# Kernel tuning notes

Measured on AMD Instinct MI355X. Metric: run time of the kernel, lower is better.

The kernel has to match this reference:

```python
import jax, jax.numpy as jnp
import numpy as np

NUM_HEADS = 16
EMBED_DIM = 2048
MAX_SEQ = 2048
HEAD_SIZE = EMBED_DIM // NUM_HEADS  # 128
ROPE_BASE = 10000.0


def setup_inputs() -> dict:
    key = jax.random.key(0)
    k1, k2, k3 = jax.random.split(key, 3)
    B, S = 4, 2048
    x = jax.random.normal(k1, (B, S, EMBED_DIM), dtype=jnp.float32)
    positions = jnp.arange(S, dtype=jnp.int32)
    # causal boolean mask: query i may attend to key j iff j <= i
    mask = jnp.tril(jnp.ones((S, MAX_SEQ), dtype=bool))[None, None]
    Wqkv = jax.random.normal(k2, (EMBED_DIM, 3 * EMBED_DIM), dtype=jnp.float32) * 0.02
    Wout = jax.random.normal(k3, (EMBED_DIM, EMBED_DIM), dtype=jnp.float32) * 0.02
    return {"x": x, "positions": positions, "mask": mask, "Wqkv": Wqkv, "Wout": Wout}


def _rope(x, positions):
    # x: [B, S, H, hd]; rotate interleaved (even, odd) pairs in last dim
    inv_freq = 1.0 / (ROPE_BASE ** (jnp.arange(0, HEAD_SIZE, 2, dtype=jnp.float32) / HEAD_SIZE))
    freq = positions.astype(jnp.float32)[:, None] * inv_freq[None, :]  # [S, hd/2]
    cos = jnp.cos(freq)[None, :, None, :]  # [1, S, 1, hd/2]
    sin = jnp.sin(freq)[None, :, None, :]
    xp = x.reshape(*x.shape[:-1], HEAD_SIZE // 2, 2)
    x0, x1 = xp[..., 0], xp[..., 1]
    out = jnp.stack([x0 * cos - x1 * sin, x1 * cos + x0 * sin], axis=-1)
    return out.reshape(x.shape)


def reference(x, positions, mask, Wqkv, Wout):
    B, S, D = x.shape
    H, hd = NUM_HEADS, HEAD_SIZE
    qkv = x @ Wqkv  # [B, S, 3D]
    q, k, v = jnp.split(qkv, 3, axis=-1)
    q = q.reshape(B, S, H, hd)
    k = k.reshape(B, S, H, hd)
    v = v.reshape(B, S, H, hd)
    q = _rope(q, positions)
    k = _rope(k, positions)
    # [B, H, S, hd]
    q = q.transpose(0, 2, 1, 3)
    k = k.transpose(0, 2, 1, 3)
    v = v.transpose(0, 2, 1, 3)
    # KV-cache update: write k/v at `positions` into a zero-initialized cache
    cache_k = jnp.zeros((B, H, MAX_SEQ, hd), dtype=x.dtype)
    cache_v = jnp.zeros((B, H, MAX_SEQ, hd), dtype=x.dtype)
    k = cache_k.at[:, :, positions].set(k)
    v = cache_v.at[:, :, positions].set(v)
    scale = 1.0 / jnp.sqrt(jnp.float32(hd))
    scores = jnp.einsum('bhqd,bhkd->bhqk', q, k) * scale  # [B, H, S, MAX_SEQ]
    scores = jnp.where(mask, scores, jnp.float32(-1e30))
    attn = jax.nn.softmax(scores, axis=-1)
    y = jnp.einsum('bhqk,bhkd->bhqd', attn, v)  # [B, H, S, hd]
    y = y.transpose(0, 2, 1, 3).reshape(B, S, D)
    return y @ Wout
```

## Files before the change

kernel.cpp:

```cpp
#include <hip/hip_runtime.h>
#include <hip/hip_bf16.h>
#include <cstdint>
#include <cstddef>

constexpr int CS = 2048;
constexpr int CHD = 128;
constexpr int CD = 2048;
constexpr int CN3 = 6144;

typedef __attribute__((ext_vector_type(8))) short short8;
typedef __attribute__((ext_vector_type(4))) float f32x4;

#define GLOAD_LDS16(g, l) __builtin_amdgcn_global_load_lds( \
    (const __attribute__((address_space(1))) void*)(g),      \
    (__attribute__((address_space(3))) void*)(l), 16, 0, 0)

__device__ __forceinline__ unsigned short f2bf(float f) {
  union { float f; unsigned u; } v; v.f = f;
  unsigned r = v.u + 0x7fffu + ((v.u >> 16) & 1u);
  return (unsigned short)(r >> 16);
}
__device__ __forceinline__ float bf2f(unsigned u16) {
  union { unsigned u; float f; } v; v.u = u16 << 16;
  return v.f;
}

template <int CTRL>
__device__ __forceinline__ float fmax_dpp(float x) {
  float y = __builtin_bit_cast(float, __builtin_amdgcn_update_dpp(
      __builtin_bit_cast(int, x), __builtin_bit_cast(int, x), CTRL, 0xf, 0xf, true));
  return fmaxf(x, y);
}
__device__ __forceinline__ float redmax16(float x) {
  x = fmax_dpp<0xB1>(x);
  x = fmax_dpp<0x4E>(x);
  x = fmax_dpp<0x141>(x);
  x = fmax_dpp<0x140>(x);
  return x;
}
__device__ __forceinline__ float dpp_xor1(float x) {
  return __builtin_bit_cast(float, __builtin_amdgcn_update_dpp(
      __builtin_bit_cast(int, x), __builtin_bit_cast(int, x), 0xB1, 0xf, 0xf, true));
}

__global__ __launch_bounds__(256) void k_cvt(const float* __restrict__ in,
                                             unsigned short* __restrict__ out, int n) {
  int i = (blockIdx.x * 256 + threadIdx.x) * 8;
  if (i >= n) return;
  float4 a = *(const float4*)(in + i);
  float4 b = *(const float4*)(in + i + 4);
  short8 o;
  o[0] = (short)f2bf(a.x); o[1] = (short)f2bf(a.y);
  o[2] = (short)f2bf(a.z); o[3] = (short)f2bf(a.w);
  o[4] = (short)f2bf(b.x); o[5] = (short)f2bf(b.y);
  o[6] = (short)f2bf(b.z); o[7] = (short)f2bf(b.w);
  *(short8*)(out + i) = o;
}

__global__ __launch_bounds__(256) void k_transcvt(const float* __restrict__ in,
                                                  unsigned short* __restrict__ out,
                                                  int R, int C) {
  __shared__ float tile[32][33];
  int c0 = blockIdx.x * 32, r0 = blockIdx.y * 32;
  int tx = threadIdx.x & 31, ty = threadIdx.x >> 5;
#pragma unroll
  for (int j = 0; j < 4; ++j)
    tile[ty + 8 * j][tx] = in[(size_t)(r0 + ty + 8 * j) * C + c0 + tx];
  __syncthreads();
#pragma unroll
  for (int j = 0; j < 4; ++j)
    out[(size_t)(c0 + ty + 8 * j) * R + r0 + tx] = f2bf(tile[tx][ty + 8 * j]);
}

__global__ __launch_bounds__(256) void k_vtrans(const unsigned short* __restrict__ V,
                                                unsigned short* __restrict__ Vt) {
  __shared__ unsigned short tile[32][33];
  int s0 = blockIdx.x * 32, d0 = blockIdx.y * 32, bh = blockIdx.z;
  int tx = threadIdx.x & 31, ty = threadIdx.x >> 5;
  const unsigned short* src = V + ((size_t)bh * CS + s0) * CHD + d0;
#pragma unroll
  for (int j = 0; j < 4; ++j)
    tile[ty + 8 * j][tx] = src[(size_t)(ty + 8 * j) * CHD + tx];
  __syncthreads();
  unsigned short* dst = Vt + ((size_t)bh * CHD + d0) * CS + s0;
#pragma unroll
  for (int j = 0; j < 4; ++j)
    dst[(size_t)(ty + 8 * j) * CS + tx] = tile[tx][ty + 8 * j];
}

__global__ void k_ropetab(float2* __restrict__ tab) {
  int p = blockIdx.x, c = threadIdx.x;
  float inv = powf(10000.0f, -(float)(2 * c) / 128.0f);
  float a = (float)p * inv;
  tab[p * 64 + c] = make_float2(cosf(a), sinf(a));
}

template <int EPI>
__global__ __launch_bounds__(512, 2) void k_gemm256(
    const unsigned short* __restrict__ A,
    const unsigned short* __restrict__ Bt,
    float* __restrict__ outF,
    unsigned short* __restrict__ outQ,
    unsigned short* __restrict__ outK,
    unsigned short* __restrict__ outV,
    const int* __restrict__ positions,
    const float2* __restrict__ tab,
    int M, int N, int K, int nbn) {
  const int nwg = gridDim.x;
  const int cpx = nwg >> 3;
  const int wg = blockIdx.x;
  const int swz = (wg & 7) * cpx + (wg >> 3);
  const int bn = swz % nbn, bm = swz / nbn;

  const int t = threadIdx.x;
  const int w = t >> 6, lane = t & 63;
  const int wr = w >> 2, wc = w & 3;
  const int lr = lane & 15, lg = lane >> 4;

  __shared__ char L[131072];

  const size_t Kb = (size_t)K * 2;
  const int srl = w * 16 + (lane >> 3);
  const int sch = ((lane & 7) ^ (lane >> 3)) * 16;
  const char* gA = (const char*)A + (size_t)(bm * 256 + srl) * Kb + sch;
  const char* gB = (const char*)Bt + (size_t)(bn * 256 + srl) * Kb + sch;
  const int ldst = w * 2048 + lane * 16;

#define STAGE(BUFB, OP, HALF, J, KT)                                               \
  GLOAD_LDS16(((OP) ? gB : gA) + (size_t)((HALF) * 128 + (J) * 8) * Kb +           \
                  (size_t)(KT) * 128,                                              \
              L + (BUFB) + (OP) * 32768 + (HALF) * 16384 + (J) * 1024 + ldst)

  const int xo = lr & 7;
  const int aRow = (wr * 128 + lr) * 128;
  const int bRow = (wc * 64 + lr) * 128;
#define RDA(BUFB, MI, KH) \
  (*(const short8*)(L + (BUFB) + aRow + (MI) * 2048 + ((((KH) * 4 + lg) ^ xo) << 4)))
#define RDB(BUFB, NI, KH) \
  (*(const short8*)(L + (BUFB) + 32768 + bRow + (NI) * 2048 + ((((KH) * 4 + lg) ^ xo) << 4)))

  f32x4 acc[8][4] = {};
  const int ktiles = K >> 6;

#pragma unroll
  for (int h = 0; h < 2; ++h)
#pragma unroll
    for (int j = 0; j < 2; ++j) { STAGE(0, 0, h, j, 0); STAGE(0, 1, h, j, 0); }
  if (ktiles > 1) {
    STAGE(65536, 0, 0, 0, 1); STAGE(65536, 0, 0, 1, 1);
    asm volatile("s_waitcnt vmcnt(2)" ::: "memory");
  } else {
    asm volatile("s_waitcnt vmcnt(0)" ::: "memory");
  }
  __builtin_amdgcn_s_barrier();

  short8 afr[4][2], bfr[4][2];

#define KTILE_PHASES(CB, NB, KT, DOSTAGE)                                          \
                                              \
  _Pragma("unroll") for (int mi = 0; mi < 4; ++mi)                                 \
      _Pragma("unroll") for (int kh = 0; kh < 2; ++kh)                             \
          afr[mi][kh] = RDA(CB, mi, kh);                                           \
  _Pragma("unroll") for (int ni = 0; ni < 2; ++ni)                                 \
      _Pragma("unroll") for (int kh = 0; kh < 2; ++kh)                             \
          bfr[ni][kh] = RDB(CB, ni, kh);                                           \
  if (DOSTAGE) { STAGE(NB, 0, 1, 0, (KT) + 1); STAGE(NB, 0, 1, 1, (KT) + 1); }     \
  __builtin_amdgcn_s_setprio(1);                                                   \
  _Pragma("unroll") for (int mi = 0; mi < 4; ++mi)                                 \
      _Pragma("unroll") for (int ni = 0; ni < 2; ++ni)                             \
          _Pragma("unroll") for (int kh = 0; kh < 2; ++kh)                         \
              acc[mi][ni] = __builtin_amdgcn_mfma_f32_16x16x32_bf16(               \
                  afr[mi][kh], bfr[ni][kh], acc[mi][ni], 0, 0, 0);                 \
  __builtin_amdgcn_s_setprio(0);                                                   \
                                                     \
  _Pragma("unroll") for (int ni = 2; ni < 4; ++ni)                                 \
      _Pragma("unroll") for (int kh = 0; kh < 2; ++kh)                             \
          bfr[ni][kh] = RDB(CB, ni, kh);                                           \
  if (DOSTAGE) { STAGE(NB, 1, 0, 0, (KT) + 1); STAGE(NB, 1, 0, 1, (KT) + 1); }     \
  __builtin_amdgcn_s_setprio(1);                                                   \
  _Pragma("unroll") for (int mi = 0; mi < 4; ++mi)                                 \
      _Pragma("unroll") for (int ni = 2; ni < 4; ++ni)                             \
          _Pragma("unroll") for (int kh = 0; kh < 2; ++kh)                         \
              acc[mi][ni] = __builtin_amdgcn_mfma_f32_16x16x32_bf16(               \
                  afr[mi][kh], bfr[ni][kh], acc[mi][ni], 0, 0, 0);                 \
  __builtin_amdgcn_s_setprio(0);                                                   \
                                                    \
  _Pragma("unroll") for (int mi = 0; mi < 4; ++mi)                                 \
      _Pragma("unroll") for (int kh = 0; kh < 2; ++kh)                             \
          afr[mi][kh] = RDA(CB, mi + 4, kh);                                       \
  if (DOSTAGE) { STAGE(NB, 1, 1, 0, (KT) + 1); STAGE(NB, 1, 1, 1, (KT) + 1); }     \
  __builtin_amdgcn_s_setprio(1);                                                   \
  _Pragma("unroll") for (int mi = 0; mi < 4; ++mi)                                 \
      _Pragma("unroll") for (int ni = 2; ni < 4; ++ni)                             \
          _Pragma("unroll") for (int kh = 0; kh < 2; ++kh)                         \
              acc[mi + 4][ni] = __builtin_amdgcn_mfma_f32_16x16x32_bf16(           \
                  afr[mi][kh], bfr[ni][kh], acc[mi + 4][ni], 0, 0, 0);             \
  __builtin_amdgcn_s_setprio(0);                                                   \
                                                       \
  __builtin_amdgcn_s_setprio(1);                                                   \
  _Pragma("unroll") for (int mi = 0; mi < 4; ++mi)                                 \
      _Pragma("unroll") for (int ni = 0; ni < 2; ++ni)                             \
          _Pragma("unroll") for (int kh = 0; kh < 2; ++kh)                         \
              acc[mi + 4][ni] = __builtin_amdgcn_mfma_f32_16x16x32_bf16(           \
                  afr[mi][kh], bfr[ni][kh], acc[mi + 4][ni], 0, 0, 0);             \
  __builtin_amdgcn_s_setprio(0);

  int c = 0;
  for (int kt = 0; kt < ktiles - 1; ++kt) {
    const int cb = c << 16, nb = (c ^ 1) << 16;
    KTILE_PHASES(cb, nb, kt, true)
    __builtin_amdgcn_s_barrier();
    if (kt + 2 < ktiles) {
      STAGE(cb, 0, 0, 0, kt + 2); STAGE(cb, 0, 0, 1, kt + 2);
      asm volatile("s_waitcnt vmcnt(2)" ::: "memory");
    } else {
      asm volatile("s_waitcnt vmcnt(0)" ::: "memory");
    }
    __builtin_amdgcn_s_barrier();
    c ^= 1;
  }
  {
    const int cb = c << 16, nb = 0;
    KTILE_PHASES(cb, nb, 0, false)
  }
#undef KTILE_PHASES
#undef STAGE
#undef RDA
#undef RDB

  if constexpr (EPI == 0) {
    const int which = bn >> 3;
    if (which < 2) {
      const float qsc = which ? 1.0f : 0.08838834764831845f;
      unsigned short* dstB = which ? outK : outQ;
#pragma unroll
      for (int mi = 0; mi < 8; ++mi)
#pragma unroll
        for (int rr = 0; rr < 4; ++rr) {
          int mg = bm * 256 + wr * 128 + mi * 16 + lg * 4 + rr;
          int bb = mg >> 11, s = mg & 2047;
          int pos = positions[s];
          int srow2 = which ? pos : s;
          const float2* tb = tab + pos * 64 + wc * 32 + (lr >> 1);
#pragma unroll
          for (int ni = 0; ni < 4; ++ni) {
            int cn = bn * 256 + wc * 64 + ni * 16 + lr;
            int h = (cn >> 7) & 15, d = cn & 127;
            float x = acc[mi][ni][rr];
            float p = dpp_xor1(x);
            float2 cs = tb[ni * 8];
            float y = (lr & 1) ? (x * cs.x + p * cs.y)
                               : (x * cs.x - p * cs.y);
            dstB[((size_t)(bb * 16 + h) * CS + srow2) * CHD + d] = f2bf(y * qsc);
          }
        }
    } else {
#pragma unroll
      for (int mi = 0; mi < 8; ++mi)
#pragma unroll
        for (int rr = 0; rr < 4; ++rr) {
          int mg = bm * 256 + wr * 128 + mi * 16 + lg * 4 + rr;
          int bb = mg >> 11, s = mg & 2047;
          int srow2 = positions[s];
#pragma unroll
          for (int ni = 0; ni < 4; ++ni) {
            int cn = bn * 256 + wc * 64 + ni * 16 + lr;
            int h = (cn >> 7) & 15, d = cn & 127;
            outV[((size_t)(bb * 16 + h) * CS + srow2) * CHD + d] = f2bf(acc[mi][ni][rr]);
          }
        }
    }
  } else {
#pragma unroll
    for (int mi = 0; mi < 8; ++mi)
#pragma unroll
      for (int rr = 0; rr < 4; ++rr) {
        int mg = bm * 256 + wr * 128 + mi * 16 + lg * 4 + rr;
#pragma unroll
        for (int ni = 0; ni < 4; ++ni)
          outF[(size_t)mg * N + bn * 256 + wc * 64 + ni * 16 + lr] = acc[mi][ni][rr];
      }
  }
}

__global__ __launch_bounds__(256, 3) void k_attn(
    const unsigned short* __restrict__ Q,
    const unsigned short* __restrict__ Kc,
    const unsigned short* __restrict__ Vt,
    unsigned short* __restrict__ Y) {
  const int qt_h = 15 - (blockIdx.x >> 6);
  const int bh = blockIdx.x & 63;
  const int q0 = qt_h * 128;
  const int t = threadIdx.x;
  const int w = t >> 6, lane = t & 63;
  const int lr = lane & 15, lg = lane >> 4;
  const int b = bh >> 4, h = bh & 15;

  __shared__ unsigned short lK[2][32 * 128];
  __shared__ unsigned short lVt[2][128 * 32];
  __shared__ unsigned short lP[4][32 * 40];

  const char* kg = (const char*)(Kc + (size_t)bh * CS * CHD);
  const char* vtg = (const char*)(Vt + (size_t)bh * CHD * CS);

  short8 qf[2][4];
#pragma unroll
  for (int qt = 0; qt < 2; ++qt)
#pragma unroll
    for (int ks = 0; ks < 4; ++ks)
      qf[qt][ks] = *(const short8*)(Q + ((size_t)bh * CS + q0 + w * 32 + qt * 16 + lr) * CHD + ks * 32 + lg * 8);

  f32x4 accy[2][8] = {};
  f32x4 accl[2] = {};
  float m[2][4];
#pragma unroll
  for (int qt = 0; qt < 2; ++qt)
#pragma unroll
    for (int r = 0; r < 4; ++r) m[qt][r] = -1e30f;

  short8 vone;
  {
    short o16 = (lr == 0) ? (short)0x3F80 : (short)0;
#pragma unroll
    for (int e = 0; e < 8; ++e) vone[e] = o16;
  }

  const int nch = 4 * qt_h + 4;
  const int qmaxw = q0 + w * 32 + 31;

  auto stage = [&](int ch) {
    const int kv0 = ch * 32;
    char* dK = (char*)lK[ch & 1];
    char* dV = (char*)lVt[ch & 1];
#pragma unroll
    for (int i = 0; i < 2; ++i) {
      int kr = w * 8 + i * 4 + lg;
      GLOAD_LDS16(kg + (size_t)(kv0 + kr) * 256 + ((lr * 16) ^ ((kr & 7) << 4)),
                  dK + w * 2048 + i * 1024 + lane * 16);
    }
#pragma unroll
    for (int i = 0; i < 2; ++i) {
      int vd = w * 32 + i * 16 + (lane >> 2);
      GLOAD_LDS16(vtg + (size_t)vd * 4096 + (size_t)kv0 * 2 + (lane & 3) * 16,
                  dV + w * 2048 + i * 1024 + lane * 16);
    }
  };

  stage(0);
  for (int ch = 0; ch < nch; ++ch) {
    __syncthreads();
    if (ch + 1 < nch) stage(ch + 1);

    const int kv0 = ch * 32;
    const unsigned short* bK = lK[ch & 1];
    const unsigned short* bV = lVt[ch & 1];

    if (kv0 <= qmaxw) {
      f32x4 sv[2][2] = {};
#pragma unroll
      for (int kvt = 0; kvt < 2; ++kvt) {
        short8 kf[4];
#pragma unroll
        for (int ks = 0; ks < 4; ++ks) {
          int row = kvt * 16 + lr;
          kf[ks] = *(const short8*)((const char*)bK + row * 256 + ((ks * 64 + lg * 16) ^ ((row & 7) << 4)));
        }
#pragma unroll
        for (int qt = 0; qt < 2; ++qt)
#pragma unroll
          for (int ks = 0; ks < 4; ++ks)
            sv[qt][kvt] = __builtin_amdgcn_mfma_f32_16x16x32_bf16(qf[qt][ks], kf[ks], sv[qt][kvt], 0, 0, 0);
      }
      float s0a[2][4], s1a[2][4], pm[2][4];
      bool need = false;
#pragma unroll
      for (int qt = 0; qt < 2; ++qt)
#pragma unroll
        for (int r = 0; r < 4; ++r) {
          const int qi = q0 + w * 32 + qt * 16 + lg * 4 + r;
          float s0 = (kv0 + lr <= qi) ? sv[qt][0][r] : -1e30f;
          float s1 = (kv0 + 16 + lr <= qi) ? sv[qt][1][r] : -1e30f;
          s0a[qt][r] = s0; s1a[qt][r] = s1;
          float mx = redmax16(fmaxf(s0, s1));
          pm[qt][r] = mx;
          need = need || (mx > m[qt][r] + 8.0f);
        }
      if (__any((int)need)) {
#pragma unroll
        for (int qt = 0; qt < 2; ++qt)
#pragma unroll
          for (int r = 0; r < 4; ++r) {
            float nm = fmaxf(m[qt][r], pm[qt][r]);
            float fr = __expf(m[qt][r] - nm);
            m[qt][r] = nm;
#pragma unroll
            for (int dt = 0; dt < 8; ++dt) accy[qt][dt][r] *= fr;
            accl[qt][r] *= fr;
          }
      }
      unsigned short* lp = lP[w];
#pragma unroll
      for (int qt = 0; qt < 2; ++qt)
#pragma unroll
        for (int r = 0; r < 4; ++r) {
          float p0 = __expf(s0a[qt][r] - m[qt][r]);
          float p1 = __expf(s1a[qt][r] - m[qt][r]);
          int prow = qt * 16 + lg * 4 + r;
          lp[prow * 40 + lr] = f2bf(p0);
          lp[prow * 40 + 16 + lr] = f2bf(p1);
        }
      short8 pa[2];
#pragma unroll
      for (int qt = 0; qt < 2; ++qt)
        pa[qt] = *(const short8*)(lp + (qt * 16 + lr) * 40 + lg * 8);
#pragma unroll
      for (int dt = 0; dt < 8; ++dt) {
        short8 vf = *(const short8*)((const char*)bV + (dt * 16 + lr) * 64 + lg * 16);
#pragma unroll
        for (int qt = 0; qt < 2; ++qt)
          accy[qt][dt] = __builtin_amdgcn_mfma_f32_16x16x32_bf16(pa[qt], vf, accy[qt][dt], 0, 0, 0);
      }
#pragma unroll
      for (int qt = 0; qt < 2; ++qt)
        accl[qt] = __builtin_amdgcn_mfma_f32_16x16x32_bf16(pa[qt], vone, accl[qt], 0, 0, 0);
    }
  }

#pragma unroll
  for (int qt = 0; qt < 2; ++qt)
#pragma unroll
    for (int r = 0; r < 4; ++r) {
      float lsum = accl[qt][r];
      lsum = __shfl(lsum, lane & 48, 64);
      float inv = 1.0f / lsum;
      int qrow = q0 + w * 32 + qt * 16 + lg * 4 + r;
      unsigned short* yr = Y + ((size_t)(b * CS + qrow)) * CD + h * CHD;
#pragma unroll
      for (int dt = 0; dt < 8; ++dt)
        yr[dt * 16 + lr] = f2bf(accy[qt][dt][r] * inv);
    }
}

extern "C" void kernel_launch(void* const* d_in, const int* in_sizes, int n_in,
                              void* d_out, int out_size, void* d_ws, size_t ws_size,
                              hipStream_t stream) {
  const float* x = (const float*)d_in[0];
  const int* positions = (const int*)d_in[1];
  const float* Wqkv = (const float*)d_in[3];
  const float* Wout = (const float*)d_in[4];
  float* out = (float*)d_out;

  char* ws = (char*)d_ws;
  size_t off = 0;
  auto alloc = [&](size_t bytes) {
    char* p = ws + off;
    off += (bytes + 255) & ~(size_t)255;
    return p;
  };
  unsigned short* q_bf = (unsigned short*)alloc((size_t)64 * CS * CHD * 2);
  unsigned short* k_bf = (unsigned short*)alloc((size_t)64 * CS * CHD * 2);
  unsigned short* v_bf = (unsigned short*)alloc((size_t)64 * CS * CHD * 2);
  unsigned short* xw = (unsigned short*)alloc((size_t)8192 * CD * 2);
  unsigned short* wT = (unsigned short*)alloc((size_t)CN3 * CD * 2);
  float2* tab = (float2*)alloc((size_t)CS * 64 * sizeof(float2));


  k_cvt<<<8192, 256, 0, stream>>>(x, xw, 8192 * CD);
  k_transcvt<<<dim3(CN3 / 32, CD / 32), 256, 0, stream>>>(Wqkv, wT, CD, CN3);
  k_ropetab<<<CS, 64, 0, stream>>>(tab);
  k_gemm256<0><<<768, 512, 0, stream>>>(xw, wT, nullptr, q_bf, k_bf, v_bf,
                                        positions, tab, 8192, CN3, CD, 24);
  k_transcvt<<<dim3(CD / 32, CD / 32), 256, 0, stream>>>(Wout, wT, CD, CD);
  k_vtrans<<<dim3(CS / 32, CHD / 32, 64), 256, 0, stream>>>(v_bf, xw);
  k_attn<<<1024, 256, 0, stream>>>(q_bf, k_bf, xw, v_bf);
  k_gemm256<1><<<256, 512, 0, stream>>>(v_bf, wT, out, nullptr, nullptr, nullptr,
                                        nullptr, nullptr, 8192, CD, CD, 8);
}
```

Before: 456.3 us.

## Compute transposed scores and build P operand via lane shuffles instead of LDS

The QK^T MFMA operands are swapped so that each lane holds scores for one query row across several keys. The row max then needs only two cross-lane shuffles instead of a 16-lane DPP reduction, and only one running max per query tile is kept. The probability matrix is packed into bf16 pairs and redistributed into the PV A-operand layout with __shfl, which removes the per-wave LDS scratch buffer and its store/load round trip. Rescale factors are transposed back to the accumulator layout with ds_bpermute. This adds eight shuffles per tile and more bpermute traffic in exchange for less LDS traffic and a smaller LDS footprint.

```diff
diff --git a/kernel.cpp b/kernel.cpp
--- a/kernel.cpp
+++ b/kernel.cpp
@@ -10,6 +10,7 @@
 
 typedef __attribute__((ext_vector_type(8))) short short8;
 typedef __attribute__((ext_vector_type(4))) float f32x4;
+typedef __attribute__((ext_vector_type(4))) int int4v;
 
 #define GLOAD_LDS16(g, l) __builtin_amdgcn_global_load_lds( \
     (const __attribute__((address_space(1))) void*)(g),      \
@@ -20,24 +21,10 @@
   unsigned r = v.u + 0x7fffu + ((v.u >> 16) & 1u);
   return (unsigned short)(r >> 16);
 }
-__device__ __forceinline__ float bf2f(unsigned u16) {
-  union { unsigned u; float f; } v; v.u = u16 << 16;
-  return v.f;
-}
-
-template <int CTRL>
-__device__ __forceinline__ float fmax_dpp(float x) {
-  float y = __builtin_bit_cast(float, __builtin_amdgcn_update_dpp(
-      __builtin_bit_cast(int, x), __builtin_bit_cast(int, x), CTRL, 0xf, 0xf, true));
-  return fmaxf(x, y);
-}
-__device__ __forceinline__ float redmax16(float x) {
-  x = fmax_dpp<0xB1>(x);
-  x = fmax_dpp<0x4E>(x);
-  x = fmax_dpp<0x141>(x);
-  x = fmax_dpp<0x140>(x);
-  return x;
-}
+__device__ __forceinline__ unsigned pkbf(float a, float b) {
+  return (unsigned)f2bf(a) | ((unsigned)f2bf(b) << 16);
+}
+
 __device__ __forceinline__ float dpp_xor1(float x) {
   return __builtin_bit_cast(float, __builtin_amdgcn_update_dpp(
       __builtin_bit_cast(int, x), __builtin_bit_cast(int, x), 0xB1, 0xf, 0xf, true));
@@ -298,7 +285,6 @@
 
   __shared__ unsigned short lK[2][32 * 128];
   __shared__ unsigned short lVt[2][128 * 32];
-  __shared__ unsigned short lP[4][32 * 40];
 
   const char* kg = (const char*)(Kc + (size_t)bh * CS * CHD);
   const char* vtg = (const char*)(Vt + (size_t)bh * CHD * CS);
@@ -312,11 +298,7 @@
 
   f32x4 accy[2][8] = {};
   f32x4 accl[2] = {};
-  float m[2][4];
-#pragma unroll
-  for (int qt = 0; qt < 2; ++qt)
-#pragma unroll
-    for (int r = 0; r < 4; ++r) m[qt][r] = -1e30f;
+  float m[2] = {-1e30f, -1e30f};
 
   short8 vone;
   {
@@ -369,50 +351,83 @@
         for (int qt = 0; qt < 2; ++qt)
 #pragma unroll
           for (int ks = 0; ks < 4; ++ks)
-            sv[qt][kvt] = __builtin_amdgcn_mfma_f32_16x16x32_bf16(qf[qt][ks], kf[ks], sv[qt][kvt], 0, 0, 0);
-      }
-      float s0a[2][4], s1a[2][4], pm[2][4];
+            sv[qt][kvt] = __builtin_amdgcn_mfma_f32_16x16x32_bf16(kf[ks], qf[qt][ks], sv[qt][kvt], 0, 0, 0);
+      }
+
+      float p8[2][8];
+      float pm[2];
       bool need = false;
 #pragma unroll
-      for (int qt = 0; qt < 2; ++qt)
-#pragma unroll
-        for (int r = 0; r < 4; ++r) {
-          const int qi = q0 + w * 32 + qt * 16 + lg * 4 + r;
-          float s0 = (kv0 + lr <= qi) ? sv[qt][0][r] : -1e30f;
-          float s1 = (kv0 + 16 + lr <= qi) ? sv[qt][1][r] : -1e30f;
-          s0a[qt][r] = s0; s1a[qt][r] = s1;
-          float mx = redmax16(fmaxf(s0, s1));
-          pm[qt][r] = mx;
-          need = need || (mx > m[qt][r] + 8.0f);
+      for (int qt = 0; qt < 2; ++qt) {
+        const int qi = q0 + w * 32 + qt * 16 + lr;
+        float mx = -1e30f;
+#pragma unroll
+        for (int kvt = 0; kvt < 2; ++kvt)
+#pragma unroll
+          for (int r = 0; r < 4; ++r) {
+            int kv = kv0 + kvt * 16 + lg * 4 + r;
+            float s = (kv <= qi) ? sv[qt][kvt][r] : -1e30f;
+            p8[qt][kvt * 4 + r] = s;
+            mx = fmaxf(mx, s);
+          }
+        mx = fmaxf(mx, __shfl_xor(mx, 32, 64));
+        mx = fmaxf(mx, __shfl_xor(mx, 16, 64));
+        pm[qt] = mx;
+        need = need || (mx > m[qt] + 8.0f);
+      }
+
+      if (__any((int)need)) {
+#pragma unroll
+        for (int qt = 0; qt < 2; ++qt) {
+          float nm = fmaxf(m[qt], pm[qt]);
+          float fr = __expf(m[qt] - nm);
+          m[qt] = nm;
+#pragma unroll
+          for (int r = 0; r < 4; ++r) {
+            int idx = (((lane >> 4) << 2) + r) << 2;
+            float frT = __builtin_bit_cast(float,
+                __builtin_amdgcn_ds_bpermute(idx, __builtin_bit_cast(int, fr)));
+#pragma unroll
+            for (int dt = 0; dt < 8; ++dt) accy[qt][dt][r] *= frT;
+            accl[qt][r] *= frT;
+          }
         }
-      if (__any((int)need)) {
-#pragma unroll
-        for (int qt = 0; qt < 2; ++qt)
-#pragma unroll
-          for (int r = 0; r < 4; ++r) {
-            float nm = fmaxf(m[qt][r], pm[qt][r]);
-            float fr = __expf(m[qt][r] - nm);
-            m[qt][r] = nm;
-#pragma unroll
-            for (int dt = 0; dt < 8; ++dt) accy[qt][dt][r] *= fr;
-            accl[qt][r] *= fr;
-          }
-      }
-      unsigned short* lp = lP[w];
-#pragma unroll
-      for (int qt = 0; qt < 2; ++qt)
-#pragma unroll
-        for (int r = 0; r < 4; ++r) {
-          float p0 = __expf(s0a[qt][r] - m[qt][r]);
-          float p1 = __expf(s1a[qt][r] - m[qt][r]);
-          int prow = qt * 16 + lg * 4 + r;
-          lp[prow * 40 + lr] = f2bf(p0);
-          lp[prow * 40 + 16 + lr] = f2bf(p1);
-        }
+      }
+
       short8 pa[2];
-#pragma unroll
-      for (int qt = 0; qt < 2; ++qt)
-        pa[qt] = *(const short8*)(lp + (qt * 16 + lr) * 40 + lg * 8);
+      const int sA = lr + ((lane & 16) << 1);
+      const int sB = sA + 16;
+      const bool hi = (lane >= 32);
+#pragma unroll
+      for (int qt = 0; qt < 2; ++qt) {
+        float pe0 = __expf(p8[qt][0] - m[qt]);
+        float pe1 = __expf(p8[qt][1] - m[qt]);
+        float pe2 = __expf(p8[qt][2] - m[qt]);
+        float pe3 = __expf(p8[qt][3] - m[qt]);
+        float pe4 = __expf(p8[qt][4] - m[qt]);
+        float pe5 = __expf(p8[qt][5] - m[qt]);
+        float pe6 = __expf(p8[qt][6] - m[qt]);
+        float pe7 = __expf(p8[qt][7] - m[qt]);
+        unsigned w0 = pkbf(pe0, pe1);
+        unsigned w1 = pkbf(pe2, pe3);
+        unsigned w2 = pkbf(pe4, pe5);
+        unsigned w3 = pkbf(pe6, pe7);
+        unsigned a0 = (unsigned)__shfl((int)w0, sA, 64);
+        unsigned a2 = (unsigned)__shfl((int)w2, sA, 64);
+        unsigned b0 = (unsigned)__shfl((int)w1, sA, 64);
+        unsigned b2 = (unsigned)__shfl((int)w3, sA, 64);
+        unsigned c0 = (unsigned)__shfl((int)w0, sB, 64);
+        unsigned c2 = (unsigned)__shfl((int)w2, sB, 64);
+        unsigned d0 = (unsigned)__shfl((int)w1, sB, 64);
+        unsigned d2 = (unsigned)__shfl((int)w3, sB, 64);
+        int4v xi;
+        xi[0] = (int)(hi ? a2 : a0);
+        xi[1] = (int)(hi ? b2 : b0);
+        xi[2] = (int)(hi ? c2 : c0);
+        xi[3] = (int)(hi ? d2 : d0);
+        pa[qt] = __builtin_bit_cast(short8, xi);
+      }
+
 #pragma unroll
       for (int dt = 0; dt < 8; ++dt) {
         short8 vf = *(const short8*)((const char*)bV + (dt * 16 + lr) * 64 + lg * 16);
```

Result: faster. 427.2 us (-6.4%).
